# Kernel optimization log

Measured on AMD Instinct MI355X. Metric: run time of the kernel, lower is better.

Reference implementation:

```python
import jax, jax.numpy as jnp
import numpy as np

HIDDEN = 1024
N_EXPERTS = 8
CAP_FACTOR = 1.1
LN_EPS = 1e-5


def setup_inputs() -> dict:
    key = jax.random.key(0)
    ks = jax.random.split(key, 8)
    d, E, dff = HIDDEN, N_EXPERTS, 4 * HIDDEN
    x = jax.random.normal(ks[0], (4, 2048, d), dtype=jnp.float32)
    gate_w = jax.random.normal(ks[1], (d, E), dtype=jnp.float32) / np.sqrt(d)
    ln_g = jnp.ones((E, d), dtype=jnp.float32)
    ln_b = jnp.zeros((E, d), dtype=jnp.float32)
    w1 = jax.random.normal(ks[2], (E, d, dff), dtype=jnp.float32) / np.sqrt(d)
    b1 = jnp.zeros((E, dff), dtype=jnp.float32)
    w2 = jax.random.normal(ks[3], (E, dff, d), dtype=jnp.float32) / np.sqrt(dff)
    b2 = jnp.zeros((E, d), dtype=jnp.float32)
    return {"x": x, "gate_w": gate_w, "ln_g": ln_g, "ln_b": ln_b,
            "w1": w1, "b1": b1, "w2": w2, "b2": b2}


def reference(x, gate_w, ln_g, ln_b, w1, b1, w2, b2):
    B, S, d = x.shape
    E = gate_w.shape[1]
    N = B * S
    cap = int(N / E * CAP_FACTOR)  # expert capacity

    xt = x.reshape(N, d)
    # Router: top-1 expert per token (max-subtract before softmax is a no-op)
    logits = xt @ gate_w                               # [N, E]
    probs = jax.nn.softmax(logits, axis=-1)
    eidx = jnp.argmax(probs, axis=-1)                  # [N] int

    onehot = jax.nn.one_hot(eidx, E, dtype=jnp.int32)  # [N, E]
    counts = onehot.sum(axis=0).astype(jnp.float32)    # pre-drop counts [E]

    # Deterministic capacity: keep first `cap` tokens per expert, drop rest.
    # (torch code drops randomly via multinomial; structure is identical.)
    pos = jnp.cumsum(onehot, axis=0) - 1               # [N, E]
    pos_tok = jnp.take_along_axis(pos, eidx[:, None], axis=1)[:, 0]  # [N]
    keep = (pos_tok < cap).astype(x.dtype)             # [N]
    pos_c = jnp.minimum(pos_tok, cap - 1)              # clamp; dropped tokens write zeros

    # Dispatch into per-expert buffers [E, cap, d]
    buf = jnp.zeros((E, cap, d), dtype=x.dtype).at[eidx, pos_c].add(xt * keep[:, None])

    # Per-expert FFN: LayerNorm -> Linear -> GELU -> Linear
    mu = buf.mean(axis=-1, keepdims=True)
    var = jnp.mean((buf - mu) ** 2, axis=-1, keepdims=True)
    nb = (buf - mu) * jax.lax.rsqrt(var + LN_EPS)
    nb = nb * ln_g[:, None, :] + ln_b[:, None, :]
    h = jax.nn.gelu(jnp.einsum('ecd,edf->ecf', nb, w1) + b1[:, None, :], approximate=False)
    y = jnp.einsum('ecf,efd->ecd', h, w2) + b2[:, None, :]  # [E, cap, d]

    # Combine: dropped tokens get zeros (matches torch output init)
    out_tok = y[eidx, pos_c] * keep[:, None]           # [N, d]
    output = out_tok.reshape(B, S, d)

    # Load-balancing loss: 1 - cosine(counts, uniform) * 0.01
    tokens_per_expert = N / E
    uniform = jnp.full((E,), tokens_per_expert, dtype=jnp.float32)
    cos = jnp.dot(counts, uniform) / (jnp.linalg.norm(counts) * jnp.linalg.norm(uniform) + 1e-8)
    loss = 1.0 - cos * 0.01
    return output, loss
```

## Files before the change

### kernel.cpp

```cpp
#include <hip/hip_runtime.h>
#include <cstdint>
#include <cstddef>

#define NTOK 8192
#define D    1024
#define DFF  4096
#define NEXP 8
#define CAP  1126
#define MPAD 1152

typedef float f32x4 __attribute__((ext_vector_type(4)));
typedef __bf16 bf16x8 __attribute__((ext_vector_type(8)));

__device__ inline unsigned short f2bf(float f) {
    unsigned u = __float_as_uint(f);
    u += 0x7fffu + ((u >> 16) & 1u);
    return (unsigned short)(u >> 16);
}

__device__ inline float gelu(float x) {
    float z  = 0.70710678118654752f * x;
    float az = fabsf(z);
    float t  = 1.0f / fmaf(0.3275911f, az, 1.0f);
    float p  = t * fmaf(t, fmaf(t, fmaf(t, fmaf(t, 1.061405429f, -1.453152027f),
                                        1.421413741f), -0.284496736f), 0.254829592f);
    float ee = __expf(-az * az);
    float er = fmaf(-p, ee, 1.0f);
    er = __builtin_copysignf(er, z);
    return 0.5f * x * (1.0f + er);
}

__device__ inline void gload16(const void* g, void* l) {
    __builtin_amdgcn_global_load_lds(
        (const __attribute__((address_space(1))) unsigned int*)g,
        (__attribute__((address_space(3))) unsigned int*)l,
        16, 0, 0);
}

__device__ void transpose_tile_dev(const float* __restrict__ W, unsigned short* __restrict__ WT,
                                   int K, int N, int tb, char* smem)
{
    int tiles_k = K >> 7, tiles_n = N >> 7;
    int per_e = tiles_k * tiles_n;
    int e = tb / per_e, rem = tb % per_e;
    int kb = rem % tiles_k, nb = rem / tiles_k;
    const float* We = W + (size_t)e * K * N + (size_t)(kb * 128) * N + nb * 128;
    unsigned short* Oe = WT + (size_t)e * K * N + (size_t)(nb * 128) * K + kb * 128;
    float* lds = (float*)smem;
    int t = threadIdx.x;
    #pragma unroll
    for (int p = 0; p < 2; ++p) {
        __syncthreads();
        #pragma unroll
        for (int j = 0; j < 8; ++j) {
            int idx = j * 256 + t;
            int r = idx >> 5, c4 = idx & 31;
            const float4 v = *(const float4*)(We + (size_t)(p * 64 + r) * N + c4 * 4);
            *(float4*)(lds + r * 128 + c4 * 4) = v;
        }
        __syncthreads();
        int c = t >> 1, half = t & 1;
        const float* col = lds + (half * 32) * 128 + c;
        unsigned short* orow = Oe + (size_t)c * K + p * 64 + half * 32;
        #pragma unroll
        for (int q = 0; q < 4; ++q) {
            uint4 o;
            o.x = f2bf(col[(q*8+0)*128]) | ((unsigned)f2bf(col[(q*8+1)*128]) << 16);
            o.y = f2bf(col[(q*8+2)*128]) | ((unsigned)f2bf(col[(q*8+3)*128]) << 16);
            o.z = f2bf(col[(q*8+4)*128]) | ((unsigned)f2bf(col[(q*8+5)*128]) << 16);
            o.w = f2bf(col[(q*8+6)*128]) | ((unsigned)f2bf(col[(q*8+7)*128]) << 16);
            *(uint4*)(orow + q * 8) = o;
        }
    }
}

__global__ __launch_bounds__(256) void transpose_kernel(
    const float* __restrict__ W, unsigned short* __restrict__ WT, int K, int N)
{
    __shared__ __align__(16) char smem[32768];
    transpose_tile_dev(W, WT, K, N, blockIdx.x, smem);
}

__global__ __launch_bounds__(256) void router_kernel(
    const float* __restrict__ x, const float* __restrict__ gw, int* __restrict__ eidx)
{
    int tok  = blockIdx.x * 4 + (threadIdx.x >> 6);
    int lane = threadIdx.x & 63;
    const float* xr = x + (size_t)tok * D;
    float a[8] = {0.f,0.f,0.f,0.f,0.f,0.f,0.f,0.f};
    #pragma unroll
    for (int it = 0; it < D / 64; ++it) {
        int d = lane + it * 64;
        float xv = xr[d];
        const float4 g0 = *(const float4*)(gw + (size_t)d * 8);
        const float4 g1 = *(const float4*)(gw + (size_t)d * 8 + 4);
        a[0] += xv * g0.x; a[1] += xv * g0.y; a[2] += xv * g0.z; a[3] += xv * g0.w;
        a[4] += xv * g1.x; a[5] += xv * g1.y; a[6] += xv * g1.z; a[7] += xv * g1.w;
    }
    #pragma unroll
    for (int off = 32; off > 0; off >>= 1)
        #pragma unroll
        for (int e = 0; e < 8; ++e) a[e] += __shfl_xor(a[e], off, 64);
    if (lane == 0) {
        int bi = 0; float bv = a[0];
        #pragma unroll
        for (int e = 1; e < 8; ++e) if (a[e] > bv) { bv = a[e]; bi = e; }
        eidx[tok] = bi;
    }
}

__global__ __launch_bounds__(1024) void scan_kernel(
    const int* __restrict__ eidx, int* __restrict__ slot_map,
    int* __restrict__ kept_cnt, float* __restrict__ loss_out,
    int* __restrict__ droplist, int* __restrict__ dropcnt)
{
    __shared__ int sc[8][1024];
    __shared__ int dcnt;
    int t = threadIdx.x;
    if (t == 0) dcnt = 0;
    int le[8];
    int c[8] = {0,0,0,0,0,0,0,0};
    #pragma unroll
    for (int i = 0; i < 8; ++i) { le[i] = eidx[t * 8 + i]; c[le[i]]++; }
    int v[8];
    #pragma unroll
    for (int e = 0; e < 8; ++e) { v[e] = c[e]; sc[e][t] = v[e]; }
    __syncthreads();
    for (int s = 1; s < 1024; s <<= 1) {
        int add[8] = {0,0,0,0,0,0,0,0};
        if (t >= s) {
            #pragma unroll
            for (int e = 0; e < 8; ++e) add[e] = sc[e][t - s];
        }
        __syncthreads();
        #pragma unroll
        for (int e = 0; e < 8; ++e) { v[e] += add[e]; sc[e][t] = v[e]; }
        __syncthreads();
    }
    int base[8];
    #pragma unroll
    for (int e = 0; e < 8; ++e) base[e] = v[e] - c[e];
    #pragma unroll
    for (int i = 0; i < 8; ++i) {
        int e = le[i]; int pos = base[e]++;
        if (pos < CAP) slot_map[e * CAP + pos] = t * 8 + i;
        else { int s = atomicAdd(&dcnt, 1); droplist[s] = t * 8 + i; }
    }
    __syncthreads();
    if (t == 0) *dropcnt = dcnt;
    if (t == 1023) {
        float dotv = 0.f, ss = 0.f;
        #pragma unroll
        for (int e = 0; e < 8; ++e) {
            float cf = (float)v[e];
            kept_cnt[e] = v[e] < CAP ? v[e] : CAP;
            dotv += cf * 1024.0f;
            ss   += cf * cf;
        }
        float denom = sqrtf(ss) * (1024.0f * sqrtf(8.0f)) + 1e-8f;
        loss_out[0] = 1.0f - 0.01f * (dotv / denom);
    }
}

__global__ __launch_bounds__(256) void zero_dropped(
    const int* __restrict__ droplist, const int* __restrict__ dropcnt,
    float4* __restrict__ out)
{
    int n = (*dropcnt) * 256;
    for (int idx = blockIdx.x * 256 + threadIdx.x; idx < n; idx += gridDim.x * 256)
        out[(size_t)droplist[idx >> 8] * 256 + (idx & 255)] = make_float4(0.f,0.f,0.f,0.f);
}

__global__ __launch_bounds__(256) void zero_out(float4* __restrict__ p, int n)
{
    int stride = gridDim.x * blockDim.x;
    for (int i = blockIdx.x * blockDim.x + threadIdx.x; i < n; i += stride)
        p[i] = make_float4(0.f, 0.f, 0.f, 0.f);
}

__global__ __launch_bounds__(256) void dispatch_ln(
    const float* __restrict__ x, const float* __restrict__ lng, const float* __restrict__ lnb,
    const int* __restrict__ slot_map, const int* __restrict__ kept_cnt,
    unsigned short* __restrict__ xbuf)
{
    int p = blockIdx.x, e = blockIdx.y, tid = threadIdx.x;
    ushort4* dst = (ushort4*)(xbuf + ((size_t)e * MPAD + p) * D) + tid;
    if (p >= kept_cnt[e]) { *dst = make_ushort4(0, 0, 0, 0); return; }
    int tok = slot_map[e * CAP + p];
    const float4 xv = *((const float4*)(x + (size_t)tok * D) + tid);
    float s  = xv.x + xv.y + xv.z + xv.w;
    float ss = xv.x * xv.x + xv.y * xv.y + xv.z * xv.z + xv.w * xv.w;
    #pragma unroll
    for (int off = 32; off > 0; off >>= 1) {
        s  += __shfl_xor(s,  off, 64);
        ss += __shfl_xor(ss, off, 64);
    }
    __shared__ float red[8];
    int lane = tid & 63, wv = tid >> 6;
    if (lane == 0) { red[wv] = s; red[4 + wv] = ss; }
    __syncthreads();
    s  = red[0] + red[1] + red[2] + red[3];
    ss = red[4] + red[5] + red[6] + red[7];
    float mu = s * (1.0f / D);
    float rs = rsqrtf(ss * (1.0f / D) - mu * mu + 1e-5f);
    const float4 gv = *((const float4*)(lng + (size_t)e * D) + tid);
    const float4 bv = *((const float4*)(lnb + (size_t)e * D) + tid);
    ushort4 o;
    o.x = f2bf((xv.x - mu) * rs * gv.x + bv.x);
    o.y = f2bf((xv.y - mu) * rs * gv.y + bv.y);
    o.z = f2bf((xv.z - mu) * rs * gv.z + bv.z);
    o.w = f2bf((xv.w - mu) * rs * gv.w + bv.w);
    *dst = o;
}

template<int K, int N, int MODE>
__global__ __launch_bounds__(256, 2) void gemm_kernel(
    const unsigned short* __restrict__ A,
    const unsigned short* __restrict__ BT,
    const float* __restrict__ bias,
    unsigned short* __restrict__ Hout,
    float* __restrict__ Yout,
    const int* __restrict__ slot_map,
    const int* __restrict__ kept_cnt,
    const float* __restrict__ tW,
    unsigned short* __restrict__ tWT,
    int tK, int tN, int tcount)
{
    __shared__ __align__(16) char smem[32768];

    if (blockIdx.x < tcount) {
        transpose_tile_dev(tW, tWT, tK, tN, blockIdx.x, smem);
        return;
    }
    const int obid = blockIdx.x - tcount;

    constexpr int MB = MPAD / 128;
    constexpr int NB = N / 128;
    constexpr int GB = NEXP * MB * NB;
    const int q8 = GB >> 3, r8 = GB & 7;
    const int xcd = obid & 7, ii = obid >> 3;
    const int swz = (xcd < r8 ? xcd * (q8 + 1) : r8 * (q8 + 1) + (xcd - r8) * q8) + ii;
    const int mb = swz % MB;
    const int t2 = swz / MB;
    const int nb = t2 % NB;
    const int e  = t2 / NB;

    const int tid  = threadIdx.x;
    const int lane = tid & 63;
    const int l15  = lane & 15, lg = lane >> 4;
    const int wave = tid >> 6, wr = wave >> 1, wc = wave & 1;
    const unsigned short* Ae = A + ((size_t)e * MPAD + (size_t)mb * 128) * K;
    const unsigned short* Be = BT + ((size_t)e * N + (size_t)nb * 128) * K;
    f32x4 acc[4][4] = {};

    auto stage = [&](int buf, int kk) {
        char* sA = smem + buf * 16384;
        char* sB = sA + 8192;
        #pragma unroll
        for (int q = 0; q < 2; ++q) {
            int cid = q * 256 + tid;
            int row = cid >> 2, pp = cid & 3;
            int cc  = pp ^ ((row >> 1) & 3);
            gload16(Ae + (size_t)row * K + kk * 32 + cc * 8, sA + cid * 16);
            gload16(Be + (size_t)row * K + kk * 32 + cc * 8, sB + cid * 16);
        }
    };
    auto compute = [&](int buf) {
        const char* sA = smem + buf * 16384;
        const char* sB = sA + 8192;
        bf16x8 af[4], bfr[4];
        #pragma unroll
        for (int i = 0; i < 4; ++i) {
            int ra = wr * 64 + i * 16 + l15;
            af[i]  = *(const bf16x8*)(sA + ra * 64 + ((lg ^ ((ra >> 1) & 3)) << 4));
            int rb = wc * 64 + i * 16 + l15;
            bfr[i] = *(const bf16x8*)(sB + rb * 64 + ((lg ^ ((rb >> 1) & 3)) << 4));
        }
        #pragma unroll
        for (int mi = 0; mi < 4; ++mi)
            #pragma unroll
            for (int ni = 0; ni < 4; ++ni)
                acc[mi][ni] = __builtin_amdgcn_mfma_f32_16x16x32_bf16(
                    bfr[ni], af[mi], acc[mi][ni], 0, 0, 0);
    };

    stage(0, 0);
    asm volatile("s_waitcnt vmcnt(0)" ::: "memory");
    __syncthreads();
    int cur = 0;
    for (int kk = 0; kk + 1 < K / 32; ++kk) {
        stage(cur ^ 1, kk + 1);
        compute(cur);
        asm volatile("s_waitcnt vmcnt(0)" ::: "memory");
        __syncthreads();
        cur ^= 1;
    }
    compute(cur);

    const int kept = (MODE == 1) ? kept_cnt[e] : 0;
    #pragma unroll
    for (int mi = 0; mi < 4; ++mi) {
        const int row = mb * 128 + wr * 64 + mi * 16 + l15;
        int tok = 0; bool live = true;
        if (MODE == 1) {
            live = row < kept;
            tok = live ? slot_map[e * CAP + row] : 0;
        }
        #pragma unroll
        for (int ni = 0; ni < 4; ++ni) {
            const int colb = nb * 128 + wc * 64 + ni * 16 + 4 * lg;
            const float4 bv = *(const float4*)(bias + (size_t)e * N + colb);
            if (MODE == 0) {
                ushort4 o;
                o.x = f2bf(gelu(acc[mi][ni][0] + bv.x));
                o.y = f2bf(gelu(acc[mi][ni][1] + bv.y));
                o.z = f2bf(gelu(acc[mi][ni][2] + bv.z));
                o.w = f2bf(gelu(acc[mi][ni][3] + bv.w));
                *(ushort4*)(Hout + ((size_t)e * MPAD + row) * N + colb) = o;
            } else if (live) {
                float4 o = make_float4(acc[mi][ni][0] + bv.x, acc[mi][ni][1] + bv.y,
                                       acc[mi][ni][2] + bv.z, acc[mi][ni][3] + bv.w);
                *(float4*)(Yout + (size_t)tok * D + colb) = o;
            }
        }
    }
}

extern "C" void kernel_launch(void* const* d_in, const int* in_sizes, int n_in,
                              void* d_out, int out_size, void* d_ws, size_t ws_size,
                              hipStream_t stream)
{
    const float* x   = (const float*)d_in[0];
    const float* gw  = (const float*)d_in[1];
    const float* lng = (const float*)d_in[2];
    const float* lnb = (const float*)d_in[3];
    const float* w1  = (const float*)d_in[4];
    const float* b1  = (const float*)d_in[5];
    const float* w2  = (const float*)d_in[6];
    const float* b2  = (const float*)d_in[7];
    float* out = (float*)d_out;
    char* ws = (char*)d_ws;

    constexpr int GB1 = NEXP * (MPAD / 128) * (DFF / 128);
    constexpr int GB2 = NEXP * (MPAD / 128) * (D / 128);
    constexpr int TB  = 2048;

    const bool fuse = (ws_size >= 228626432ULL);

    if (fuse) {
        unsigned short* wT1  = (unsigned short*)ws;
        unsigned short* wT2  = (unsigned short*)(ws + 67108864);
        int* eidx     = (int*)wT2;
        int* droplist = (int*)wT2 + NTOK;
        unsigned short* xbuf = (unsigned short*)(ws + 134217728);
        unsigned short* hbuf = (unsigned short*)(ws + 153092096);
        int* slot_map = (int*)(ws + 228589568);
        int* kept     = slot_map + NEXP * CAP;
        int* dropcnt  = kept + NEXP;

        router_kernel<<<NTOK / 4, 256, 0, stream>>>(x, gw, eidx);
        scan_kernel<<<1, 1024, 0, stream>>>(eidx, slot_map, kept,
                                            out + (size_t)NTOK * D, droplist, dropcnt);
        zero_dropped<<<64, 256, 0, stream>>>(droplist, dropcnt, (float4*)out);
        dispatch_ln<<<dim3(MPAD, NEXP), 256, 0, stream>>>(x, lng, lnb, slot_map, kept, xbuf);

        transpose_kernel<<<TB, 256, 0, stream>>>(w1, wT1, D, DFF);
        gemm_kernel<D, DFF, 0><<<TB + GB1, 256, 0, stream>>>(
            xbuf, wT1, b1, hbuf, nullptr, slot_map, kept, w2, wT2, DFF, D, TB);
        gemm_kernel<DFF, D, 1><<<GB2, 256, 0, stream>>>(
            hbuf, wT2, b2, nullptr, out, slot_map, kept, nullptr, nullptr, 0, 0, 0);
    } else {
        unsigned short* wT   = (unsigned short*)ws;
        unsigned short* xbuf = (unsigned short*)(ws + 67108864);
        unsigned short* hbuf = (unsigned short*)(ws + 67108864 + 18874368);
        int* eidx     = (int*)(ws + 161480704);
        int* slot_map = eidx + NTOK;
        int* kept     = slot_map + NEXP * CAP;
        int* dropcnt  = kept + NEXP;
        int* droplist = (int*)hbuf;

        router_kernel<<<NTOK / 4, 256, 0, stream>>>(x, gw, eidx);
        scan_kernel<<<1, 1024, 0, stream>>>(eidx, slot_map, kept,
                                            out + (size_t)NTOK * D, droplist, dropcnt);
        zero_out<<<2048, 256, 0, stream>>>((float4*)out, NTOK * D / 4);
        dispatch_ln<<<dim3(MPAD, NEXP), 256, 0, stream>>>(x, lng, lnb, slot_map, kept, xbuf);

        transpose_kernel<<<TB, 256, 0, stream>>>(w1, wT, D, DFF);
        gemm_kernel<D, DFF, 0><<<GB1, 256, 0, stream>>>(
            xbuf, wT, b1, hbuf, nullptr, slot_map, kept, nullptr, nullptr, 0, 0, 0);
        transpose_kernel<<<TB, 256, 0, stream>>>(w2, wT, DFF, D);
        gemm_kernel<DFF, D, 1><<<GB2, 256, 0, stream>>>(
            hbuf, wT, b2, nullptr, out, slot_map, kept, nullptr, nullptr, 0, 0, 0);
    }
}
```

Before: 344.2 us.

## Double GEMM K-tile to 64 and drop fused transpose path

The GEMM's K step grows from 32 to 64, with a wider 8-way XOR swizzle and two MFMA sub-steps per stage. This halves the number of barriers and load/compute iterations but doubles LDS use to 64 KB, which may cut occupancy. The large-workspace path that hid the w2 transpose inside the first GEMM launch is removed, so both transposes now run as separate kernels. The full-output zero_out is replaced by zeroing only the dropped tokens.

New measurement: 344.9 us. Within noise of the previous version (+0.2%).

```diff
diff --git a/kernel.cpp b/kernel.cpp
--- a/kernel.cpp
+++ b/kernel.cpp
@@ -169,13 +169,6 @@
     int n = (*dropcnt) * 256;
     for (int idx = blockIdx.x * 256 + threadIdx.x; idx < n; idx += gridDim.x * 256)
         out[(size_t)droplist[idx >> 8] * 256 + (idx & 255)] = make_float4(0.f,0.f,0.f,0.f);
-}
-
-__global__ __launch_bounds__(256) void zero_out(float4* __restrict__ p, int n)
-{
-    int stride = gridDim.x * blockDim.x;
-    for (int i = blockIdx.x * blockDim.x + threadIdx.x; i < n; i += stride)
-        p[i] = make_float4(0.f, 0.f, 0.f, 0.f);
 }
 
 __global__ __launch_bounds__(256) void dispatch_ln(
@@ -221,22 +214,14 @@
     unsigned short* __restrict__ Hout,
     float* __restrict__ Yout,
     const int* __restrict__ slot_map,
-    const int* __restrict__ kept_cnt,
-    const float* __restrict__ tW,
-    unsigned short* __restrict__ tWT,
-    int tK, int tN, int tcount)
-{
-    __shared__ __align__(16) char smem[32768];
-
-    if (blockIdx.x < tcount) {
-        transpose_tile_dev(tW, tWT, tK, tN, blockIdx.x, smem);
-        return;
-    }
-    const int obid = blockIdx.x - tcount;
-
+    const int* __restrict__ kept_cnt)
+{
     constexpr int MB = MPAD / 128;
     constexpr int NB = N / 128;
     constexpr int GB = NEXP * MB * NB;
+    __shared__ __align__(16) char smem[65536];
+
+    const int obid = blockIdx.x;
     const int q8 = GB >> 3, r8 = GB & 7;
     const int xcd = obid & 7, ii = obid >> 3;
     const int swz = (xcd < r8 ? xcd * (q8 + 1) : r8 * (q8 + 1) + (xcd - r8) * q8) + ii;
@@ -254,41 +239,49 @@
     f32x4 acc[4][4] = {};
 
     auto stage = [&](int buf, int kk) {
-        char* sA = smem + buf * 16384;
-        char* sB = sA + 8192;
-        #pragma unroll
-        for (int q = 0; q < 2; ++q) {
+        char* sA = smem + buf * 32768;
+        char* sB = sA + 16384;
+        #pragma unroll
+        for (int q = 0; q < 4; ++q) {
             int cid = q * 256 + tid;
-            int row = cid >> 2, pp = cid & 3;
-            int cc  = pp ^ ((row >> 1) & 3);
-            gload16(Ae + (size_t)row * K + kk * 32 + cc * 8, sA + cid * 16);
-            gload16(Be + (size_t)row * K + kk * 32 + cc * 8, sB + cid * 16);
+            int row = cid >> 3, pp = cid & 7;
+            int cc  = pp ^ ((row >> 1) & 7);
+            gload16(Ae + (size_t)row * K + kk * 64 + cc * 8, sA + cid * 16);
+            gload16(Be + (size_t)row * K + kk * 64 + cc * 8, sB + cid * 16);
         }
     };
     auto compute = [&](int buf) {
-        const char* sA = smem + buf * 16384;
-        const char* sB = sA + 8192;
-        bf16x8 af[4], bfr[4];
-        #pragma unroll
-        for (int i = 0; i < 4; ++i) {
-            int ra = wr * 64 + i * 16 + l15;
-            af[i]  = *(const bf16x8*)(sA + ra * 64 + ((lg ^ ((ra >> 1) & 3)) << 4));
-            int rb = wc * 64 + i * 16 + l15;
-            bfr[i] = *(const bf16x8*)(sB + rb * 64 + ((lg ^ ((rb >> 1) & 3)) << 4));
-        }
-        #pragma unroll
-        for (int mi = 0; mi < 4; ++mi)
+        const char* sA = smem + buf * 32768;
+        const char* sB = sA + 16384;
+        bf16x8 af[2][4], bfr[2][4];
+        #pragma unroll
+        for (int ks = 0; ks < 2; ++ks) {
             #pragma unroll
-            for (int ni = 0; ni < 4; ++ni)
-                acc[mi][ni] = __builtin_amdgcn_mfma_f32_16x16x32_bf16(
-                    bfr[ni], af[mi], acc[mi][ni], 0, 0, 0);
+            for (int i = 0; i < 4; ++i) {
+                int ra = wr * 64 + i * 16 + l15;
+                af[ks][i]  = *(const bf16x8*)(sA + ra * 128 +
+                             (((ks * 4 + lg) ^ ((ra >> 1) & 7)) << 4));
+                int rb = wc * 64 + i * 16 + l15;
+                bfr[ks][i] = *(const bf16x8*)(sB + rb * 128 +
+                             (((ks * 4 + lg) ^ ((rb >> 1) & 7)) << 4));
+            }
+        }
+        #pragma unroll
+        for (int ks = 0; ks < 2; ++ks)
+            #pragma unroll
+            for (int mi = 0; mi < 4; ++mi)
+                #pragma unroll
+                for (int ni = 0; ni < 4; ++ni)
+                    acc[mi][ni] = __builtin_amdgcn_mfma_f32_16x16x32_bf16(
+                        bfr[ks][ni], af[ks][mi], acc[mi][ni], 0, 0, 0);
     };
 
+    constexpr int T = K / 64;
     stage(0, 0);
     asm volatile("s_waitcnt vmcnt(0)" ::: "memory");
     __syncthreads();
     int cur = 0;
-    for (int kk = 0; kk + 1 < K / 32; ++kk) {
+    for (int kk = 0; kk + 1 < T; ++kk) {
         stage(cur ^ 1, kk + 1);
         compute(cur);
         asm volatile("s_waitcnt vmcnt(0)" ::: "memory");
@@ -341,55 +334,31 @@
     float* out = (float*)d_out;
     char* ws = (char*)d_ws;
 
+    unsigned short* wT   = (unsigned short*)ws;
+    unsigned short* xbuf = (unsigned short*)(ws + 67108864);
+    unsigned short* hbuf = (unsigned short*)(ws + 67108864 + 18874368);
+    int* eidx     = (int*)(ws + 161480704);
+    int* slot_map = eidx + NTOK;
+    int* kept     = slot_map + NEXP * CAP;
+    int* dropcnt  = kept + NEXP;
+    int* droplist = dropcnt + 8;
+
     constexpr int GB1 = NEXP * (MPAD / 128) * (DFF / 128);
     constexpr int GB2 = NEXP * (MPAD / 128) * (D / 128);
-    constexpr int TB  = 2048;
-
-    const bool fuse = (ws_size >= 228626432ULL);
-
-    if (fuse) {
-        unsigned short* wT1  = (unsigned short*)ws;
-        unsigned short* wT2  = (unsigned short*)(ws + 67108864);
-        int* eidx     = (int*)wT2;
-        int* droplist = (int*)wT2 + NTOK;
-        unsigned short* xbuf = (unsigned short*)(ws + 134217728);
-        unsigned short* hbuf = (unsigned short*)(ws + 153092096);
-        int* slot_map = (int*)(ws + 228589568);
-        int* kept     = slot_map + NEXP * CAP;
-        int* dropcnt  = kept + NEXP;
-
-        router_kernel<<<NTOK / 4, 256, 0, stream>>>(x, gw, eidx);
-        scan_kernel<<<1, 1024, 0, stream>>>(eidx, slot_map, kept,
-                                            out + (size_t)NTOK * D, droplist, dropcnt);
-        zero_dropped<<<64, 256, 0, stream>>>(droplist, dropcnt, (float4*)out);
-        dispatch_ln<<<dim3(MPAD, NEXP), 256, 0, stream>>>(x, lng, lnb, slot_map, kept, xbuf);
-
-        transpose_kernel<<<TB, 256, 0, stream>>>(w1, wT1, D, DFF);
-        gemm_kernel<D, DFF, 0><<<TB + GB1, 256, 0, stream>>>(
-            xbuf, wT1, b1, hbuf, nullptr, slot_map, kept, w2, wT2, DFF, D, TB);
-        gemm_kernel<DFF, D, 1><<<GB2, 256, 0, stream>>>(
-            hbuf, wT2, b2, nullptr, out, slot_map, kept, nullptr, nullptr, 0, 0, 0);
-    } else {
-        unsigned short* wT   = (unsigned short*)ws;
-        unsigned short* xbuf = (unsigned short*)(ws + 67108864);
-        unsigned short* hbuf = (unsigned short*)(ws + 67108864 + 18874368);
-        int* eidx     = (int*)(ws + 161480704);
-        int* slot_map = eidx + NTOK;
-        int* kept     = slot_map + NEXP * CAP;
-        int* dropcnt  = kept + NEXP;
-        int* droplist = (int*)hbuf;
-
-        router_kernel<<<NTOK / 4, 256, 0, stream>>>(x, gw, eidx);
-        scan_kernel<<<1, 1024, 0, stream>>>(eidx, slot_map, kept,
-                                            out + (size_t)NTOK * D, droplist, dropcnt);
-        zero_out<<<2048, 256, 0, stream>>>((float4*)out, NTOK * D / 4);
-        dispatch_ln<<<dim3(MPAD, NEXP), 256, 0, stream>>>(x, lng, lnb, slot_map, kept, xbuf);
-
-        transpose_kernel<<<TB, 256, 0, stream>>>(w1, wT, D, DFF);
-        gemm_kernel<D, DFF, 0><<<GB1, 256, 0, stream>>>(
-            xbuf, wT, b1, hbuf, nullptr, slot_map, kept, nullptr, nullptr, 0, 0, 0);
-        transpose_kernel<<<TB, 256, 0, stream>>>(w2, wT, DFF, D);
-        gemm_kernel<DFF, D, 1><<<GB2, 256, 0, stream>>>(
-            hbuf, wT, b2, nullptr, out, slot_map, kept, nullptr, nullptr, 0, 0, 0);
-    }
-}
+    constexpr int TB1 = NEXP * (D / 128) * (DFF / 128);
+    constexpr int TB2 = NEXP * (DFF / 128) * (D / 128);
+
+    router_kernel<<<NTOK / 4, 256, 0, stream>>>(x, gw, eidx);
+    scan_kernel<<<1, 1024, 0, stream>>>(eidx, slot_map, kept,
+                                        out + (size_t)NTOK * D, droplist, dropcnt);
+    zero_dropped<<<64, 256, 0, stream>>>(droplist, dropcnt, (float4*)out);
+    dispatch_ln<<<dim3(MPAD, NEXP), 256, 0, stream>>>(x, lng, lnb, slot_map, kept, xbuf);
+
+    transpose_kernel<<<TB1, 256, 0, stream>>>(w1, wT, D, DFF);
+    gemm_kernel<D, DFF, 0><<<GB1, 256, 0, stream>>>(
+        xbuf, wT, b1, hbuf, nullptr, slot_map, kept);
+
+    transpose_kernel<<<TB2, 256, 0, stream>>>(w2, wT, DFF, D);
+    gemm_kernel<DFF, D, 1><<<GB2, 256, 0, stream>>>(
+        hbuf, wT, b2, nullptr, out, slot_map, kept);
+}
```
